# Kernel optimization log

Hardware: AMD Instinct MI355X
Metric: run time of the kernel (lower is better)

The kernel has to match this reference:

```python
import jax, jax.numpy as jnp
import numpy as np

D_INNER = 5120
DT_RANK = 160
N_STATE = 16
BATCH = 256


def _softplus_thresh20(x):
    # ttnn.softplus(parameter1=1.0, parameter2=20.0): linear above threshold 20
    return jnp.where(x > 20.0, x, jnp.log1p(jnp.exp(jnp.minimum(x, 20.0))))


def setup_inputs() -> dict:
    key = jax.random.key(0)
    ks = jax.random.split(key, 9)
    x = jax.random.normal(ks[0], (1, 1, BATCH, D_INNER), dtype=jnp.float32)
    # scale weights by 1/sqrt(fan_in) so softplus input is O(1)
    W_dt_low = jax.random.normal(ks[1], (D_INNER, DT_RANK), dtype=jnp.float32) / np.sqrt(D_INNER)
    W_dt = jax.random.normal(ks[2], (DT_RANK, D_INNER), dtype=jnp.float32) / np.sqrt(DT_RANK)
    b_dt = jax.random.normal(ks[3], (D_INNER,), dtype=jnp.float32)
    W_B = jax.random.normal(ks[4], (D_INNER, N_STATE), dtype=jnp.float32) / np.sqrt(D_INNER)
    W_C = jax.random.normal(ks[5], (D_INNER, N_STATE), dtype=jnp.float32) / np.sqrt(D_INNER)
    # A = -exp(A_log): strictly negative, as in the module's preprocess_A
    A = -jnp.exp(0.5 * jax.random.normal(ks[6], (D_INNER, N_STATE), dtype=jnp.float32))
    D = jax.random.normal(ks[7], (D_INNER,), dtype=jnp.float32)
    h0 = 0.1 * jax.random.normal(ks[8], (BATCH, D_INNER, N_STATE), dtype=jnp.float32)
    return {"x": x, "W_dt_low": W_dt_low, "W_dt": W_dt, "b_dt": b_dt,
            "W_B": W_B, "W_C": W_C, "A": A, "D": D, "h0": h0}


def reference(x, W_dt_low, W_dt, b_dt, W_B, W_C, A, D, h0):
    b, d = x.shape[2], x.shape[3]
    xb = x.reshape(b, d)                                  # (B, D)
    # delta = softplus(x @ x_proj_dt @ dt_proj + bias)
    delta = _softplus_thresh20(xb @ W_dt_low @ W_dt + b_dt)   # (B, D)
    Bp = xb @ W_B                                         # (B, N)
    Cp = xb @ W_C                                         # (B, N)
    # discretize: abar = exp(delta * A), bbar = delta * B
    # layout (B, D, N) matches repeat_interleave(delta, n) / repeat(B, d)
    abar = jnp.exp(delta[:, :, None] * A[None, :, :])     # (B, D, N)
    bbar = delta[:, :, None] * Bp[:, None, :]             # (B, D, N)
    h = abar * h0 + bbar * xb[:, :, None]                 # (B, D, N)
    y = jnp.einsum('bdn,bn->bd', h, Cp)                   # reduce over state
    out = xb * D[None, :] + y                             # (B, D)
    return out.reshape(1, 1, b, d)
```

## Files before the change

kernel.cpp:

```cpp
#include <hip/hip_runtime.h>
#include <math.h>

#define D_INNER 5120
#define DT_RANK 160
#define N_STATE 16
#define BATCH   256
#define KTOT    192

#define BGRP    8
#define NBG     (BATCH / BGRP)
#define DDBLK   160
#define NDDB    (D_INNER / DDBLK)
#define SPLIT   32

#define K3_BT   4

#define OFF_T     0
#define SZ_T      (BATCH * KTOT)
#define OFF_P     (OFF_T + SZ_T)
#define SZ_P      (SPLIT * BATCH * KTOT)

__global__ __launch_bounds__(256) void k1_gemm(const float* __restrict__ x,
                                               const float* __restrict__ Wdtlow,
                                               const float* __restrict__ WB,
                                               const float* __restrict__ WC,
                                               float* __restrict__ ws) {
    __shared__ float lds[4 * BGRP * KTOT];
    const int tid  = threadIdx.x;
    const int lane = tid & 63;
    const int wv   = tid >> 6;
    const int b0   = blockIdx.x * BGRP;
    const int ddB  = blockIdx.y * DDBLK;

    float* xs = lds;
    for (int j = tid; j < (BGRP * DDBLK) / 4; j += 256) {
        int i  = j / (DDBLK / 4);
        int c4 = j % (DDBLK / 4);
        float4 v = *(const float4*)(x + (size_t)(b0 + i) * D_INNER + ddB + c4 * 4);
        *(float4*)(xs + i * DDBLK + c4 * 4) = v;
    }
    __syncthreads();

    const int dd0 = wv * 40;
    const float* p0 = Wdtlow + (size_t)(ddB + dd0) * DT_RANK + lane;
    const float* p1 = p0 + 64;
    const float* p2;
    int st2;
    if (lane < 32)      { p2 = p0 + 128;                                          st2 = DT_RANK; }
    else if (lane < 48) { p2 = WB + (size_t)(ddB + dd0) * N_STATE + (lane - 32);  st2 = N_STATE; }
    else                { p2 = WC + (size_t)(ddB + dd0) * N_STATE + (lane - 48);  st2 = N_STATE; }

    float acc0[BGRP], acc1[BGRP], acc2[BGRP];
#pragma unroll
    for (int i = 0; i < BGRP; ++i) { acc0[i] = 0.f; acc1[i] = 0.f; acc2[i] = 0.f; }

#pragma unroll 2
    for (int g = 0; g < 10; ++g) {
        float w0[4], w1[4], w2[4];
#pragma unroll
        for (int u = 0; u < 4; ++u) {
            int dd = g * 4 + u;
            w0[u] = p0[(size_t)dd * DT_RANK];
            w1[u] = p1[(size_t)dd * DT_RANK];
            w2[u] = p2[(size_t)dd * st2];
        }
#pragma unroll
        for (int i = 0; i < BGRP; ++i) {
            float4 xv = *(const float4*)(xs + i * DDBLK + dd0 + g * 4);
            acc0[i] += xv.x * w0[0] + xv.y * w0[1] + xv.z * w0[2] + xv.w * w0[3];
            acc1[i] += xv.x * w1[0] + xv.y * w1[1] + xv.z * w1[2] + xv.w * w1[3];
            acc2[i] += xv.x * w2[0] + xv.y * w2[1] + xv.z * w2[2] + xv.w * w2[3];
        }
    }
    __syncthreads();

#pragma unroll
    for (int i = 0; i < BGRP; ++i) {
        float* r = lds + wv * (BGRP * KTOT) + i * KTOT;
        r[lane]       = acc0[i];
        r[lane + 64]  = acc1[i];
        r[lane + 128] = acc2[i];
    }
    __syncthreads();

    float* P = ws + OFF_P + (size_t)blockIdx.y * (BATCH * KTOT) + (size_t)b0 * KTOT;
#pragma unroll
    for (int r = 0; r < 6; ++r) {
        int idx = tid + r * 256;
        P[idx] = lds[idx] + lds[idx + 1536] + lds[idx + 3072] + lds[idx + 4608];
    }
}

__global__ __launch_bounds__(256) void k2_reduce(float* __restrict__ ws) {
    int g = blockIdx.x * 256 + threadIdx.x;
    const float* P = ws + OFF_P;
    float a = 0.f;
#pragma unroll
    for (int s = 0; s < SPLIT; ++s) a += P[(size_t)s * (BATCH * KTOT) + g];
    ws[OFF_T + g] = a;
}

__global__ __launch_bounds__(256, 6) void k3_fused(const float* __restrict__ Wdt,
                                                   const float* __restrict__ b_dt,
                                                   const float* __restrict__ x,
                                                   const float* __restrict__ A,
                                                   const float* __restrict__ Dv,
                                                   const float* __restrict__ h0,
                                                   const float* __restrict__ ws,
                                                   float* __restrict__ out) {
    const int tid = threadIdx.x;
    const int d   = blockIdx.x * 256 + tid;
    const int b0  = blockIdx.y * K3_BT;
    const float* T = ws + OFF_T;

    const float* t0 = T + (size_t)(b0 + 0) * KTOT;
    const float* t1 = T + (size_t)(b0 + 1) * KTOT;
    const float* t2 = T + (size_t)(b0 + 2) * KTOT;
    const float* t3 = T + (size_t)(b0 + 3) * KTOT;

    float acc[K3_BT] = {0.f, 0.f, 0.f, 0.f};
#pragma unroll 8
    for (int k = 0; k < DT_RANK; ++k) {
        float w = Wdt[(size_t)k * D_INNER + d];
        acc[0] += t0[k] * w;
        acc[1] += t1[k] * w;
        acc[2] += t2[k] * w;
        acc[3] += t3[k] * w;
    }

    const float bdt = b_dt[d];
    const float Dd  = Dv[d];
    const float4* a4 = (const float4*)(A + (size_t)d * N_STATE);
    float4 a0 = a4[0], a1 = a4[1], a2 = a4[2], a3 = a4[3];

    const float4* hb = (const float4*)(h0 + ((size_t)b0 * D_INNER + d) * N_STATE);
    const size_t  hstride = (size_t)D_INNER * 4;

    float4 hc0 = hb[0], hc1 = hb[1], hc2 = hb[2], hc3 = hb[3];

#pragma unroll
    for (int i = 0; i < K3_BT; ++i) {
        float4 hn0, hn1, hn2, hn3;
        if (i < K3_BT - 1) {
            const float4* hn = hb + (size_t)(i + 1) * hstride;
            hn0 = hn[0]; hn1 = hn[1]; hn2 = hn[2]; hn3 = hn[3];
        }

        const int b = b0 + i;
        const float* Tb = T + (size_t)b * KTOT;

        float v     = acc[i] + bdt;
        float delta = (v > 20.f) ? v : log1pf(__expf(v));

        float sbc = 0.f;
#pragma unroll
        for (int n = 0; n < N_STATE; ++n) sbc += Tb[160 + n] * Tb[176 + n];

        float y = 0.f;
        y += __expf(delta * a0.x) * hc0.x * Tb[176 + 0];
        y += __expf(delta * a0.y) * hc0.y * Tb[176 + 1];
        y += __expf(delta * a0.z) * hc0.z * Tb[176 + 2];
        y += __expf(delta * a0.w) * hc0.w * Tb[176 + 3];
        y += __expf(delta * a1.x) * hc1.x * Tb[176 + 4];
        y += __expf(delta * a1.y) * hc1.y * Tb[176 + 5];
        y += __expf(delta * a1.z) * hc1.z * Tb[176 + 6];
        y += __expf(delta * a1.w) * hc1.w * Tb[176 + 7];
        y += __expf(delta * a2.x) * hc2.x * Tb[176 + 8];
        y += __expf(delta * a2.y) * hc2.y * Tb[176 + 9];
        y += __expf(delta * a2.z) * hc2.z * Tb[176 + 10];
        y += __expf(delta * a2.w) * hc2.w * Tb[176 + 11];
        y += __expf(delta * a3.x) * hc3.x * Tb[176 + 12];
        y += __expf(delta * a3.y) * hc3.y * Tb[176 + 13];
        y += __expf(delta * a3.z) * hc3.z * Tb[176 + 14];
        y += __expf(delta * a3.w) * hc3.w * Tb[176 + 15];

        float xv = x[(size_t)b * D_INNER + d];
        out[(size_t)b * D_INNER + d] = xv * (Dd + delta * sbc) + y;

        if (i < K3_BT - 1) { hc0 = hn0; hc1 = hn1; hc2 = hn2; hc3 = hn3; }
    }
}

extern "C" void kernel_launch(void* const* d_in, const int* in_sizes, int n_in,
                              void* d_out, int out_size, void* d_ws, size_t ws_size,
                              hipStream_t stream) {
    const float* x      = (const float*)d_in[0];
    const float* Wdtlow = (const float*)d_in[1];
    const float* Wdt    = (const float*)d_in[2];
    const float* bdt    = (const float*)d_in[3];
    const float* WB     = (const float*)d_in[4];
    const float* WC     = (const float*)d_in[5];
    const float* A      = (const float*)d_in[6];
    const float* Dv     = (const float*)d_in[7];
    const float* h0     = (const float*)d_in[8];
    float* ws  = (float*)d_ws;
    float* out = (float*)d_out;

    hipLaunchKernelGGL(k1_gemm, dim3(NBG, NDDB), dim3(256), 0, stream,
                       x, Wdtlow, WB, WC, ws);
    hipLaunchKernelGGL(k2_reduce, dim3((BATCH * KTOT) / 256), dim3(256), 0, stream, ws);
    hipLaunchKernelGGL(k3_fused, dim3(D_INNER / 256, BATCH / K3_BT), dim3(256),
                       0, stream, Wdt, bdt, x, A, Dv, h0, ws, out);
}
```

Before: 175.2 us.

## Widen k3 batch tile, precompute B·C dot in reduce, deepen h0 prefetch

Doubles the batch rows per k3 block from 4 to 8, so each Wdt column load is reused across more batch rows, and lowers the launch-bounds occupancy hint from 6 to 4 to leave room for the extra registers. The per-batch B·C dot product moves into k2_reduce, which now runs one block per batch row and writes the result to a new workspace slot. k3 prefetches h0 two batch rows ahead, issues the x loads early, and splits the y sum into four partial accumulators to shorten the dependency chain. The main risk is register pressure and lower occupancy, and the larger tile halves the number of k3 blocks.

```diff
diff --git a/kernel.cpp b/kernel.cpp
--- a/kernel.cpp
+++ b/kernel.cpp
@@ -13,12 +13,13 @@
 #define NDDB    (D_INNER / DDBLK)
 #define SPLIT   32
 
-#define K3_BT   4
+#define K3_BT   8
 
 #define OFF_T     0
 #define SZ_T      (BATCH * KTOT)
 #define OFF_P     (OFF_T + SZ_T)
 #define SZ_P      (SPLIT * BATCH * KTOT)
+#define OFF_SBC   (OFF_P + SZ_P)
 
 __global__ __launch_bounds__(256) void k1_gemm(const float* __restrict__ x,
                                                const float* __restrict__ Wdtlow,
@@ -91,16 +92,26 @@
     }
 }
 
-__global__ __launch_bounds__(256) void k2_reduce(float* __restrict__ ws) {
-    int g = blockIdx.x * 256 + threadIdx.x;
-    const float* P = ws + OFF_P;
+__global__ __launch_bounds__(192) void k2_reduce(float* __restrict__ ws) {
+    __shared__ float ts[KTOT];
+    const int b   = blockIdx.x;
+    const int col = threadIdx.x;
+    const float* P = ws + OFF_P + (size_t)b * KTOT + col;
     float a = 0.f;
 #pragma unroll
-    for (int s = 0; s < SPLIT; ++s) a += P[(size_t)s * (BATCH * KTOT) + g];
-    ws[OFF_T + g] = a;
-}
-
-__global__ __launch_bounds__(256, 6) void k3_fused(const float* __restrict__ Wdt,
+    for (int s = 0; s < SPLIT; ++s) a += P[(size_t)s * (BATCH * KTOT)];
+    ws[OFF_T + b * KTOT + col] = a;
+    ts[col] = a;
+    __syncthreads();
+    if (col == 0) {
+        float s2 = 0.f;
+#pragma unroll
+        for (int n = 0; n < N_STATE; ++n) s2 += ts[160 + n] * ts[176 + n];
+        ws[OFF_SBC + b] = s2;
+    }
+}
+
+__global__ __launch_bounds__(256, 4) void k3_fused(const float* __restrict__ Wdt,
                                                    const float* __restrict__ b_dt,
                                                    const float* __restrict__ x,
                                                    const float* __restrict__ A,
@@ -111,39 +122,40 @@
     const int tid = threadIdx.x;
     const int d   = blockIdx.x * 256 + tid;
     const int b0  = blockIdx.y * K3_BT;
-    const float* T = ws + OFF_T;
-
-    const float* t0 = T + (size_t)(b0 + 0) * KTOT;
-    const float* t1 = T + (size_t)(b0 + 1) * KTOT;
-    const float* t2 = T + (size_t)(b0 + 2) * KTOT;
-    const float* t3 = T + (size_t)(b0 + 3) * KTOT;
-
-    float acc[K3_BT] = {0.f, 0.f, 0.f, 0.f};
-#pragma unroll 8
-    for (int k = 0; k < DT_RANK; ++k) {
-        float w = Wdt[(size_t)k * D_INNER + d];
-        acc[0] += t0[k] * w;
-        acc[1] += t1[k] * w;
-        acc[2] += t2[k] * w;
-        acc[3] += t3[k] * w;
-    }
+    const float* T  = ws + OFF_T;
+    const float* SB = ws + OFF_SBC;
+
+    const float4* hb = (const float4*)(h0 + ((size_t)b0 * D_INNER + d) * N_STATE);
+    const size_t  hstride = (size_t)D_INNER * 4;
+
+    float4 hc0 = hb[0], hc1 = hb[1], hc2 = hb[2], hc3 = hb[3];
+    const float4* h1p = hb + hstride;
+    float4 hn0 = h1p[0], hn1 = h1p[1], hn2 = h1p[2], hn3 = h1p[3];
+
+    float xv[K3_BT];
+#pragma unroll
+    for (int i = 0; i < K3_BT; ++i) xv[i] = x[(size_t)(b0 + i) * D_INNER + d];
 
     const float bdt = b_dt[d];
     const float Dd  = Dv[d];
     const float4* a4 = (const float4*)(A + (size_t)d * N_STATE);
     float4 a0 = a4[0], a1 = a4[1], a2 = a4[2], a3 = a4[3];
 
-    const float4* hb = (const float4*)(h0 + ((size_t)b0 * D_INNER + d) * N_STATE);
-    const size_t  hstride = (size_t)D_INNER * 4;
-
-    float4 hc0 = hb[0], hc1 = hb[1], hc2 = hb[2], hc3 = hb[3];
+    float acc[K3_BT] = {0.f, 0.f, 0.f, 0.f, 0.f, 0.f, 0.f, 0.f};
+#pragma unroll 4
+    for (int k = 0; k < DT_RANK; ++k) {
+        float w = Wdt[(size_t)k * D_INNER + d];
+#pragma unroll
+        for (int i = 0; i < K3_BT; ++i)
+            acc[i] += T[(size_t)(b0 + i) * KTOT + k] * w;
+    }
 
 #pragma unroll
     for (int i = 0; i < K3_BT; ++i) {
-        float4 hn0, hn1, hn2, hn3;
-        if (i < K3_BT - 1) {
-            const float4* hn = hb + (size_t)(i + 1) * hstride;
-            hn0 = hn[0]; hn1 = hn[1]; hn2 = hn[2]; hn3 = hn[3];
+        float4 p0, p1, p2, p3;
+        if (i + 2 < K3_BT) {
+            const float4* hp = hb + (size_t)(i + 2) * hstride;
+            p0 = hp[0]; p1 = hp[1]; p2 = hp[2]; p3 = hp[3];
         }
 
         const int b = b0 + i;
@@ -151,33 +163,31 @@
 
         float v     = acc[i] + bdt;
         float delta = (v > 20.f) ? v : log1pf(__expf(v));
-
-        float sbc = 0.f;
-#pragma unroll
-        for (int n = 0; n < N_STATE; ++n) sbc += Tb[160 + n] * Tb[176 + n];
-
-        float y = 0.f;
-        y += __expf(delta * a0.x) * hc0.x * Tb[176 + 0];
-        y += __expf(delta * a0.y) * hc0.y * Tb[176 + 1];
-        y += __expf(delta * a0.z) * hc0.z * Tb[176 + 2];
-        y += __expf(delta * a0.w) * hc0.w * Tb[176 + 3];
-        y += __expf(delta * a1.x) * hc1.x * Tb[176 + 4];
-        y += __expf(delta * a1.y) * hc1.y * Tb[176 + 5];
-        y += __expf(delta * a1.z) * hc1.z * Tb[176 + 6];
-        y += __expf(delta * a1.w) * hc1.w * Tb[176 + 7];
-        y += __expf(delta * a2.x) * hc2.x * Tb[176 + 8];
-        y += __expf(delta * a2.y) * hc2.y * Tb[176 + 9];
-        y += __expf(delta * a2.z) * hc2.z * Tb[176 + 10];
-        y += __expf(delta * a2.w) * hc2.w * Tb[176 + 11];
-        y += __expf(delta * a3.x) * hc3.x * Tb[176 + 12];
-        y += __expf(delta * a3.y) * hc3.y * Tb[176 + 13];
-        y += __expf(delta * a3.z) * hc3.z * Tb[176 + 14];
-        y += __expf(delta * a3.w) * hc3.w * Tb[176 + 15];
-
-        float xv = x[(size_t)b * D_INNER + d];
-        out[(size_t)b * D_INNER + d] = xv * (Dd + delta * sbc) + y;
+        float sbc   = SB[b];
+
+        float y0, y1, y2, y3;
+        y0  = __expf(delta * a0.x) * hc0.x * Tb[176 + 0];
+        y0 += __expf(delta * a0.y) * hc0.y * Tb[176 + 1];
+        y0 += __expf(delta * a0.z) * hc0.z * Tb[176 + 2];
+        y0 += __expf(delta * a0.w) * hc0.w * Tb[176 + 3];
+        y1  = __expf(delta * a1.x) * hc1.x * Tb[176 + 4];
+        y1 += __expf(delta * a1.y) * hc1.y * Tb[176 + 5];
+        y1 += __expf(delta * a1.z) * hc1.z * Tb[176 + 6];
+        y1 += __expf(delta * a1.w) * hc1.w * Tb[176 + 7];
+        y2  = __expf(delta * a2.x) * hc2.x * Tb[176 + 8];
+        y2 += __expf(delta * a2.y) * hc2.y * Tb[176 + 9];
+        y2 += __expf(delta * a2.z) * hc2.z * Tb[176 + 10];
+        y2 += __expf(delta * a2.w) * hc2.w * Tb[176 + 11];
+        y3  = __expf(delta * a3.x) * hc3.x * Tb[176 + 12];
+        y3 += __expf(delta * a3.y) * hc3.y * Tb[176 + 13];
+        y3 += __expf(delta * a3.z) * hc3.z * Tb[176 + 14];
+        y3 += __expf(delta * a3.w) * hc3.w * Tb[176 + 15];
+
+        out[(size_t)b * D_INNER + d] = xv[i] * (Dd + delta * sbc)
+                                     + ((y0 + y1) + (y2 + y3));
 
         if (i < K3_BT - 1) { hc0 = hn0; hc1 = hn1; hc2 = hn2; hc3 = hn3; }
+        if (i + 2 < K3_BT) { hn0 = p0;  hn1 = p1;  hn2 = p2;  hn3 = p3;  }
     }
 }
 
@@ -198,7 +208,7 @@
 
     hipLaunchKernelGGL(k1_gemm, dim3(NBG, NDDB), dim3(256), 0, stream,
                        x, Wdtlow, WB, WC, ws);
-    hipLaunchKernelGGL(k2_reduce, dim3((BATCH * KTOT) / 256), dim3(256), 0, stream, ws);
+    hipLaunchKernelGGL(k2_reduce, dim3(BATCH), dim3(192), 0, stream, ws);
     hipLaunchKernelGGL(k3_fused, dim3(D_INNER / 256, BATCH / K3_BT), dim3(256),
                        0, stream, Wdt, bdt, x, A, Dv, h0, ws, out);
 }
```

Measured after the change: 182.8 us. +4.3%, slower.
